# Kernel optimization log

Hardware: AMD Instinct MI355X
Metric: run time of the kernel (lower is better)

Reference implementation:

```python
import jax, jax.numpy as jnp
import numpy as np
import math

T_STEPS = 100      # diffusion steps
TED = 16           # time_embed_dim
NODE_C = 4         # node_num_classes
EDGE_C = 2         # edge_num_classes
HID = 64           # hidden_dim
H = 4              # nhead
B = 256            # graphs per batch
NPG = 64           # nodes per graph
DEG = 8            # avg out-degree
N = B * NPG
E = N * DEG
IN_CH = NODE_C + TED  # 20


def sinusoidal_embedding(t_vec, dim):
    # t_vec: [1] float. Matches get_sinusoidal_embedding for even dim.
    half = dim // 2
    scale = math.log(10000.0) / (half - 1)
    freqs = jnp.exp(-jnp.arange(half, dtype=jnp.float32) * scale)  # [half]
    emb = t_vec[:, None] * freqs[None, :]                          # [1, half]
    return jnp.concatenate([jnp.sin(emb), jnp.cos(emb)], axis=1)   # [1, dim]


def transformer_conv(x, src, dst, Wq, bq, Wk, bk, Wv, bv, Ws, bs):
    # PyG TransformerConv, concat=False (mean over heads), root_weight=True,
    # beta=False, no edge features, dropout=0 (eval).
    n = x.shape[0]
    q = (x @ Wq + bq).reshape(n, H, HID)
    k = (x @ Wk + bk).reshape(n, H, HID)
    v = (x @ Wv + bv).reshape(n, H, HID)
    # attention logits per edge, softmax over incoming edges of each dst node
    logits = jnp.sum(q[dst] * k[src], axis=-1) / math.sqrt(HID)    # [E, H]
    lmax = jax.ops.segment_max(logits, dst, num_segments=n)       # [n, H]
    ex = jnp.exp(logits - lmax[dst])                              # [E, H]
    denom = jax.ops.segment_sum(ex, dst, num_segments=n)          # [n, H]
    attn = ex / jnp.where(denom == 0, 1.0, denom)[dst]            # [E, H]
    msg = v[src] * attn[:, :, None]                               # [E, H, HID]
    agg = jax.ops.segment_sum(msg, dst, num_segments=n)           # [n, H, HID]
    return agg.mean(axis=1) + x @ Ws + bs                         # [n, HID]


def setup_inputs() -> dict:
    key = jax.random.key(0)
    ks = jax.random.split(key, 32)

    # node features: random one-hot labels
    labels = jax.random.randint(ks[0], (N,), 0, NODE_C)
    x = jax.nn.one_hot(labels, NODE_C, dtype=jnp.float32)

    # per-graph random edges (kept within each graph via offsets)
    src_l = jax.random.randint(ks[1], (B, NPG * DEG), 0, NPG)
    dst_l = jax.random.randint(ks[2], (B, NPG * DEG), 0, NPG)
    off = (jnp.arange(B) * NPG)[:, None]
    edge_index = jnp.stack([(src_l + off).reshape(-1), (dst_l + off).reshape(-1)]).astype(jnp.int64)

    batch = jnp.repeat(jnp.arange(B, dtype=jnp.int64), NPG)

    def lin(k, fin, fout):
        kw, kb = jax.random.split(k)
        W = jax.random.normal(kw, (fin, fout), jnp.float32) / math.sqrt(fin)
        b = jax.random.normal(kb, (fout,), jnp.float32) * 0.01
        return W, b

    W_time, b_time = lin(ks[3], TED, TED)
    Wq1, bq1 = lin(ks[4], IN_CH, H * HID)
    Wk1, bk1 = lin(ks[5], IN_CH, H * HID)
    Wv1, bv1 = lin(ks[6], IN_CH, H * HID)
    Ws1, bs1 = lin(ks[7], IN_CH, HID)
    Wq2, bq2 = lin(ks[8], HID, H * HID)
    Wk2, bk2 = lin(ks[9], HID, H * HID)
    Wv2, bv2 = lin(ks[10], HID, H * HID)
    Ws2, bs2 = lin(ks[11], HID, HID)
    W_node, b_node = lin(ks[12], HID, NODE_C)
    W_e1, b_e1 = lin(ks[13], 2 * HID, HID)
    W_e2, b_e2 = lin(ks[14], HID, EDGE_C)

    return dict(x=x, edge_index=edge_index, batch=batch, t=50,
                W_time=W_time, b_time=b_time,
                Wq1=Wq1, bq1=bq1, Wk1=Wk1, bk1=bk1, Wv1=Wv1, bv1=bv1, Ws1=Ws1, bs1=bs1,
                Wq2=Wq2, bq2=bq2, Wk2=Wk2, bk2=bk2, Wv2=Wv2, bv2=bv2, Ws2=Ws2, bs2=bs2,
                W_node=W_node, b_node=b_node, W_e1=W_e1, b_e1=b_e1, W_e2=W_e2, b_e2=b_e2)


def reference(x, edge_index, batch, t,
              W_time, b_time,
              Wq1, bq1, Wk1, bk1, Wv1, bv1, Ws1, bs1,
              Wq2, bq2, Wk2, bk2, Wv2, bv2, Ws2, bs2,
              W_node, b_node, W_e1, b_e1, W_e2, b_e2):
    src, dst = edge_index[0], edge_index[1]

    # time embedding: sinusoidal(t/T) -> Linear -> broadcast to all nodes
    t_vec = jnp.asarray([t], jnp.float32) / T_STEPS
    temb = sinusoidal_embedding(t_vec, TED) @ W_time + b_time      # [1, TED]
    temb = jnp.broadcast_to(temb, (x.shape[0], TED))
    x_in = jnp.concatenate([x, temb], axis=1)                      # [N, 20]

    h = jax.nn.relu(transformer_conv(x_in, src, dst, Wq1, bq1, Wk1, bk1, Wv1, bv1, Ws1, bs1))
    h = jax.nn.relu(transformer_conv(h, src, dst, Wq2, bq2, Wk2, bk2, Wv2, bv2, Ws2, bs2))

    node_logits = h @ W_node + b_node                              # [N, 4]

    # to_dense_batch with equal-sized graphs == reshape; vectorized edge MLP
    hd = h.reshape(B, NPG, HID)
    pair = jnp.concatenate([
        jnp.broadcast_to(hd[:, :, None, :], (B, NPG, NPG, HID)),
        jnp.broadcast_to(hd[:, None, :, :], (B, NPG, NPG, HID)),
    ], axis=-1)                                                    # [B, n, n, 2*HID]
    e_hidden = jax.nn.relu(pair @ W_e1 + b_e1)
    edge_logits = e_hidden @ W_e2 + b_e2                           # [B, n, n, 2]
    return node_logits, edge_logits
```

## Files before the change

kernel.cpp:

```cpp
#include <hip/hip_runtime.h>
#include <math.h>

constexpr int EPG  = 512;
constexpr int ETOT = 131072;

constexpr size_t TAB_Q  = 0;
constexpr size_t TAB_K  = 1024;
constexpr size_t TAB_V  = 2048;
constexpr size_t TAB_S  = 3072;
constexpr size_t TAB_LG = 3328;
constexpr int PK_Q_HI   = 0;
constexpr int PK_Q_LO   = 16384;
constexpr int PK_K_HI   = 32768;
constexpr int PK_K_LO   = 49152;
constexpr int PK_V_HI   = 65536;
constexpr int PK_V_LO   = 81920;
constexpr int PK_S_HI   = 98304;
constexpr int PK_S_LO   = 102400;
constexpr int PK_E1T_HI = 106496;
constexpr int PK_E1T_LO = 110592;
constexpr int PK_E1B_HI = 114688;
constexpr int PK_E1B_LO = 118784;

typedef short bf16x8 __attribute__((ext_vector_type(8)));
typedef float f32x4  __attribute__((ext_vector_type(4)));

__device__ __forceinline__ short f2bf(float x) {
    unsigned u = __float_as_uint(x);
    u = (u + 0x7fffu + ((u >> 16) & 1u)) >> 16;
    return (short)u;
}
__device__ __forceinline__ float bf2f(short h) {
    return __uint_as_float(((unsigned)(unsigned short)h) << 16);
}
__device__ __forceinline__ void splt(float x, short& hi, short& lo) {
    hi = f2bf(x);
    lo = f2bf(x - bf2f(hi));
}

__device__ __forceinline__ f32x4 mfma3(bf16x8 ah, bf16x8 al, bf16x8 bh, bf16x8 bl, f32x4 c) {
    c = __builtin_amdgcn_mfma_f32_16x16x32_bf16(ah, bh, c, 0, 0, 0);
    c = __builtin_amdgcn_mfma_f32_16x16x32_bf16(ah, bl, c, 0, 0, 0);
    c = __builtin_amdgcn_mfma_f32_16x16x32_bf16(al, bh, c, 0, 0, 0);
    return c;
}

__device__ __forceinline__ bf16x8 ldsfrag(const short* p, int rowb, int kb, int lane) {
    return *(const bf16x8*)&p[(rowb + (lane & 15)) * 72 + kb + ((lane >> 4) << 3)];
}
__device__ __forceinline__ bf16x8 gpfrag(const short* p, int colb, int kb, int lane) {
    return *(const bf16x8*)&p[((colb + (lane & 15)) << 6) + kb + ((lane >> 4) << 3)];
}

__global__ __launch_bounds__(256) void k_tables(
    const int* __restrict__ t_ptr,
    const float* __restrict__ Wt,  const float* __restrict__ bt,
    const float* __restrict__ Wq1, const float* __restrict__ bq1,
    const float* __restrict__ Wk1, const float* __restrict__ bk1,
    const float* __restrict__ Wv1, const float* __restrict__ bv1,
    const float* __restrict__ Ws1, const float* __restrict__ bs1,
    float* __restrict__ ws)
{
    __shared__ float se[16], temb[16];
    __shared__ float q1t[4][256], k1t[4][256], v1t[4][256], s1t[4][64];
    const int t = threadIdx.x;

    if (t < 8) {
        float tv = (float)(*t_ptr) * 0.01f;
        float scale = logf(10000.0f) / 7.0f;
        float e = tv * expf(-(float)t * scale);
        se[t]     = sinf(e);
        se[t + 8] = cosf(e);
    }
    __syncthreads();
    if (t < 16) {
        float acc = bt[t];
        for (int i = 0; i < 16; i++) acc += se[i] * Wt[i * 16 + t];
        temb[t] = acc;
    }
    __syncthreads();
    {
        const int o = t;
        float tq = 0.f, tk = 0.f, tv = 0.f;
        for (int d = 0; d < 16; d++) {
            float td = temb[d];
            tq += td * Wq1[(4 + d) * 256 + o];
            tk += td * Wk1[(4 + d) * 256 + o];
            tv += td * Wv1[(4 + d) * 256 + o];
        }
        for (int c = 0; c < 4; c++) {
            q1t[c][o] = Wq1[c * 256 + o] + tq + bq1[o];
            k1t[c][o] = Wk1[c * 256 + o] + tk + bk1[o];
            v1t[c][o] = Wv1[c * 256 + o] + tv + bv1[o];
        }
        if (o < 64) {
            float ts = 0.f;
            for (int d = 0; d < 16; d++) ts += temb[d] * Ws1[(4 + d) * 64 + o];
            for (int c = 0; c < 4; c++) s1t[c][o] = Ws1[c * 64 + o] + ts + bs1[o];
        }
    }
    __syncthreads();
    for (int idx = t; idx < 1024; idx += 256) {
        int c = idx >> 8, o = idx & 255;
        ws[TAB_Q + idx] = q1t[c][o];
        ws[TAB_K + idx] = k1t[c][o];
        ws[TAB_V + idx] = v1t[c][o];
    }
    ws[TAB_S + t] = s1t[t >> 6][t & 63];
    if (t < 64) {
        int cd = t >> 4, cs = (t >> 2) & 3, h = t & 3;
        float acc = 0.f;
        for (int d = 0; d < 64; d++) acc += q1t[cd][h * 64 + d] * k1t[cs][h * 64 + d];
        ws[TAB_LG + t] = acc * 0.125f;
    }
}

__global__ __launch_bounds__(256) void k_prep(
    const float* __restrict__ Wq, const float* __restrict__ Wk,
    const float* __restrict__ Wv, const float* __restrict__ Wsk,
    const float* __restrict__ We1, short* __restrict__ wsh)
{
    int b = blockIdx.x, t = threadIdx.x;
    const float* src; int N; int dhi; int nb;
    if (b < 64)       { src = Wq;           N = 256; dhi = PK_Q_HI;   nb = b; }
    else if (b < 128) { src = Wk;           N = 256; dhi = PK_K_HI;   nb = b - 64; }
    else if (b < 192) { src = Wv;           N = 256; dhi = PK_V_HI;   nb = b - 128; }
    else if (b < 208) { src = Wsk;          N = 64;  dhi = PK_S_HI;   nb = b - 192; }
    else if (b < 224) { src = We1;          N = 64;  dhi = PK_E1T_HI; nb = b - 208; }
    else              { src = We1 + 64*64;  N = 64;  dhi = PK_E1B_HI; nb = b - 224; }
    int dlo = dhi + N * 64;
    int n = nb * 4 + (t >> 6), kk = t & 63;
    float v = src[(size_t)kk * N + n];
    short hi, lo; splt(v, hi, lo);
    wsh[dhi + n * 64 + kk] = hi;
    wsh[dlo + n * 64 + kk] = lo;
}

__global__ __launch_bounds__(512) void k_main(
    const float* __restrict__ x, const int* __restrict__ ei,
    const float* __restrict__ ws, const short* __restrict__ wsh,
    const float* __restrict__ bq, const float* __restrict__ bk,
    const float* __restrict__ bv, const float* __restrict__ bsk,
    const float* __restrict__ Wn, const float* __restrict__ bn,
    const float* __restrict__ be1, const float* __restrict__ We2,
    const float* __restrict__ be2, float* __restrict__ out)
{
    __shared__ __align__(16) char smem[130304];
    short* hHi    = (short*)(smem + 0);
    short* hLo    = (short*)(smem + 9216);
    short* qHi    = (short*)(smem + 18432);
    short* qLo    = (short*)(smem + 27648);
    short* kHi    = (short*)(smem + 36864);
    short* kLo    = (short*)(smem + 46080);
    short* vtHi   = (short*)(smem + 55296);
    short* vtLo   = (short*)(smem + 64512);
    short* pHi    = (short*)(smem + 73728);
    short* pLo    = (short*)(smem + 82944);
    float* Ssf    = (float*)(smem + 92160);
    int*   Cc     = (int*)(smem + 109568);
    int*   cnt4   = (int*)(smem + 117760);
    float* alphaF = (float*)(smem + 118784);
    float* v1t    = (float*)(smem + 122880);
    float* s1t    = (float*)(smem + 126976);
    float* lgs    = (float*)(smem + 128000);
    float* WnS    = (float*)(smem + 128256);
    float* w2s    = (float*)(smem + 129280);
    float* invsf  = (float*)(smem + 129792);
    int*   cls    = (int*)(smem + 130048);
    float* Asf    = (float*)(smem + 18432);
    float* BTf    = (float*)(smem + 36864);

    const int g = blockIdx.x, t = threadIdx.x;
    const int lane = t & 63, w = t >> 6;
    const int rowb = (w & 3) * 16;
    const int ch   = w >> 2;
    const int row8 = t >> 3;
    const int d08  = (t & 7) * 8;

    for (int i = t; i < 1024; i += 512) v1t[i] = ws[TAB_V + i];
    if (t < 256) s1t[t] = ws[TAB_S + t];
    if (t < 64)  lgs[t] = ws[TAB_LG + t];
    if (t < 256) WnS[t] = Wn[t];
    if (t < 128) w2s[(t & 1) * 64 + (t >> 1)] = We2[t];
    if (t < 64) {
        const float* xr = x + (size_t)(g * 64 + t) * 4;
        int c = 0;
        if (xr[1] > 0.5f) c = 1;
        if (xr[2] > 0.5f) c = 2;
        if (xr[3] > 0.5f) c = 3;
        cls[t] = c;
    }
    if (t < 256) cnt4[t] = 0;
    for (int i = t; i < 2048; i += 512) Cc[i] = 0;
    __syncthreads();

    {
        int ge = g * EPG + t;
        int ls = ei[ge] - g * 64;
        int ld = ei[ETOT + ge] - g * 64;
        int idx = ld * 64 + ls;
        atomicAdd(&Cc[idx >> 1], 1 << ((idx & 1) * 16));
        atomicAdd(&cnt4[ld * 4 + cls[ls]], 1);
    }
    __syncthreads();

    if (t < 256) {
        int n = t >> 2, h = t & 3;
        int cd = cls[n];
        int   c[4]; float l[4];
        #pragma unroll
        for (int cc = 0; cc < 4; cc++) {
            c[cc] = cnt4[n * 4 + cc];
            l[cc] = lgs[cd * 16 + cc * 4 + h];
        }
        float m = -1e30f;
        #pragma unroll
        for (int cc = 0; cc < 4; cc++) if (c[cc] > 0) m = fmaxf(m, l[cc]);
        float e[4]; float den = 0.f;
        #pragma unroll
        for (int cc = 0; cc < 4; cc++) {
            e[cc] = (c[cc] > 0) ? (float)c[cc] * expf(l[cc] - m) : 0.f;
            den += e[cc];
        }
        float inv = (den > 0.f) ? 0.25f / den : 0.f;
        #pragma unroll
        for (int cc = 0; cc < 4; cc++) alphaF[n * 16 + h * 4 + cc] = e[cc] * inv;
    }
    __syncthreads();

    {
        int cd = cls[row8];
        float a[16];
        #pragma unroll
        for (int q = 0; q < 16; q++) a[q] = alphaF[row8 * 16 + q];
        #pragma unroll
        for (int jj = 0; jj < 8; jj++) {
            int d = d08 + jj;
            float acc = s1t[cd * 64 + d];
            #pragma unroll
            for (int h = 0; h < 4; h++)
                #pragma unroll
                for (int c = 0; c < 4; c++)
                    acc += a[h * 4 + c] * v1t[c * 256 + h * 64 + d];
            float o = fmaxf(acc, 0.f);
            short hi, lo; splt(o, hi, lo);
            hHi[row8 * 72 + d] = hi;
            hLo[row8 * 72 + d] = lo;
        }
    }
    __syncthreads();

    bf16x8 Ah0 = ldsfrag(hHi, rowb, 0, lane),  Ah1 = ldsfrag(hHi, rowb, 32, lane);
    bf16x8 Al0 = ldsfrag(hLo, rowb, 0, lane),  Al1 = ldsfrag(hLo, rowb, 32, lane);

    f32x4 skacc[2];
    #pragma unroll
    for (int ct = 0; ct < 2; ct++) {
        int colb = ch * 32 + ct * 16;
        f32x4 a = {0.f, 0.f, 0.f, 0.f};
        a = mfma3(Ah0, Al0, gpfrag(wsh + PK_S_HI, colb, 0, lane),
                             gpfrag(wsh + PK_S_LO, colb, 0, lane), a);
        a = mfma3(Ah1, Al1, gpfrag(wsh + PK_S_HI, colb, 32, lane),
                             gpfrag(wsh + PK_S_LO, colb, 32, lane), a);
        float bb = bsk[colb + (lane & 15)];
        #pragma unroll
        for (int r = 0; r < 4; r++) a[r] += bb;
        skacc[ct] = a;
    }

    float hacc[2][4] = {};
    for (int h = 0; h < 4; h++) {
        #pragma unroll
        for (int ct = 0; ct < 2; ct++) {
            int colb = ch * 32 + ct * 16;
            int gcol = h * 64 + colb;
            f32x4 qa = {0.f,0.f,0.f,0.f}, ka = {0.f,0.f,0.f,0.f}, va = {0.f,0.f,0.f,0.f};
            qa = mfma3(Ah0, Al0, gpfrag(wsh + PK_Q_HI, gcol, 0, lane),
                                  gpfrag(wsh + PK_Q_LO, gcol, 0, lane), qa);
            qa = mfma3(Ah1, Al1, gpfrag(wsh + PK_Q_HI, gcol, 32, lane),
                                  gpfrag(wsh + PK_Q_LO, gcol, 32, lane), qa);
            ka = mfma3(Ah0, Al0, gpfrag(wsh + PK_K_HI, gcol, 0, lane),
                                  gpfrag(wsh + PK_K_LO, gcol, 0, lane), ka);
            ka = mfma3(Ah1, Al1, gpfrag(wsh + PK_K_HI, gcol, 32, lane),
                                  gpfrag(wsh + PK_K_LO, gcol, 32, lane), ka);
            va = mfma3(Ah0, Al0, gpfrag(wsh + PK_V_HI, gcol, 0, lane),
                                  gpfrag(wsh + PK_V_LO, gcol, 0, lane), va);
            va = mfma3(Ah1, Al1, gpfrag(wsh + PK_V_HI, gcol, 32, lane),
                                  gpfrag(wsh + PK_V_LO, gcol, 32, lane), va);
            float bqv = bq[gcol + (lane & 15)];
            float bkv = bk[gcol + (lane & 15)];
            float bvv = bv[gcol + (lane & 15)];
            int cc = colb + (lane & 15);
            #pragma unroll
            for (int r = 0; r < 4; r++) {
                int rr = rowb + ((lane >> 4) << 2) + r;
                short hi, lo;
                splt((qa[r] + bqv) * 0.125f, hi, lo);
                qHi[rr * 72 + cc] = hi;  qLo[rr * 72 + cc] = lo;
                splt(ka[r] + bkv, hi, lo);
                kHi[rr * 72 + cc] = hi;  kLo[rr * 72 + cc] = lo;
                splt(va[r] + bvv, hi, lo);
                vtHi[cc * 72 + rr] = hi; vtLo[cc * 72 + rr] = lo;
            }
        }
        __syncthreads();

        {
            bf16x8 qh0 = ldsfrag(qHi, rowb, 0, lane),  qh1 = ldsfrag(qHi, rowb, 32, lane);
            bf16x8 ql0 = ldsfrag(qLo, rowb, 0, lane),  ql1 = ldsfrag(qLo, rowb, 32, lane);
            #pragma unroll
            for (int ct = 0; ct < 2; ct++) {
                int colb = ch * 32 + ct * 16;
                f32x4 s = {0.f, 0.f, 0.f, 0.f};
                s = mfma3(qh0, ql0, ldsfrag(kHi, colb, 0, lane),
                                     ldsfrag(kLo, colb, 0, lane), s);
                s = mfma3(qh1, ql1, ldsfrag(kHi, colb, 32, lane),
                                     ldsfrag(kLo, colb, 32, lane), s);
                int cc = colb + (lane & 15);
                #pragma unroll
                for (int r = 0; r < 4; r++)
                    Ssf[(rowb + ((lane >> 4) << 2) + r) * 68 + cc] = s[r];
            }
        }
        __syncthreads();

        {
            int cv[8]; float sv[8];
            #pragma unroll
            for (int jj = 0; jj < 8; jj++) {
                int idx = row8 * 64 + d08 + jj;
                cv[jj] = (Cc[idx >> 1] >> ((idx & 1) * 16)) & 0xffff;
                sv[jj] = Ssf[row8 * 68 + d08 + jj];
            }
            float m = -1e30f;
            #pragma unroll
            for (int jj = 0; jj < 8; jj++) if (cv[jj] > 0) m = fmaxf(m, sv[jj]);
            m = fmaxf(m, __shfl_xor(m, 1, 8));
            m = fmaxf(m, __shfl_xor(m, 2, 8));
            m = fmaxf(m, __shfl_xor(m, 4, 8));
            float den = 0.f; float p[8];
            #pragma unroll
            for (int jj = 0; jj < 8; jj++) {
                p[jj] = (cv[jj] > 0) ? (float)cv[jj] * expf(sv[jj] - m) : 0.f;
                den += p[jj];
            }
            den += __shfl_xor(den, 1, 8);
            den += __shfl_xor(den, 2, 8);
            den += __shfl_xor(den, 4, 8);
            #pragma unroll
            for (int jj = 0; jj < 8; jj++) {
                short hi, lo; splt(p[jj], hi, lo);
                pHi[row8 * 72 + d08 + jj] = hi;
                pLo[row8 * 72 + d08 + jj] = lo;
            }
            if ((t & 7) == 0) invsf[row8] = (den > 0.f) ? 1.f / den : 0.f;
        }
        __syncthreads();

        {
            bf16x8 ph0 = ldsfrag(pHi, rowb, 0, lane),  ph1 = ldsfrag(pHi, rowb, 32, lane);
            bf16x8 pl0 = ldsfrag(pLo, rowb, 0, lane),  pl1 = ldsfrag(pLo, rowb, 32, lane);
            #pragma unroll
            for (int ct = 0; ct < 2; ct++) {
                int colb = ch * 32 + ct * 16;
                f32x4 pv = {0.f, 0.f, 0.f, 0.f};
                pv = mfma3(ph0, pl0, ldsfrag(vtHi, colb, 0, lane),
                                      ldsfrag(vtLo, colb, 0, lane), pv);
                pv = mfma3(ph1, pl1, ldsfrag(vtHi, colb, 32, lane),
                                      ldsfrag(vtLo, colb, 32, lane), pv);
                #pragma unroll
                for (int r = 0; r < 4; r++)
                    hacc[ct][r] += pv[r] * invsf[rowb + ((lane >> 4) << 2) + r];
            }
        }
        __syncthreads();
    }

    #pragma unroll
    for (int ct = 0; ct < 2; ct++) {
        int colb = ch * 32 + ct * 16;
        int cc = colb + (lane & 15);
        #pragma unroll
        for (int r = 0; r < 4; r++) {
            int rr = rowb + ((lane >> 4) << 2) + r;
            float v = fmaxf(0.25f * hacc[ct][r] + skacc[ct][r], 0.f);
            short hi, lo; splt(v, hi, lo);
            hHi[rr * 72 + cc] = hi;
            hLo[rr * 72 + cc] = lo;
            Ssf[rr * 68 + cc] = v;
        }
    }
    __syncthreads();

    {
        bf16x8 ah0 = ldsfrag(hHi, rowb, 0, lane),  ah1 = ldsfrag(hHi, rowb, 32, lane);
        bf16x8 al0 = ldsfrag(hLo, rowb, 0, lane),  al1 = ldsfrag(hLo, rowb, 32, lane);
        #pragma unroll
        for (int ct = 0; ct < 2; ct++) {
            int colb = ch * 32 + ct * 16;
            f32x4 aa = {0.f,0.f,0.f,0.f}, bb2 = {0.f,0.f,0.f,0.f};
            aa  = mfma3(ah0, al0, gpfrag(wsh + PK_E1T_HI, colb, 0, lane),
                                   gpfrag(wsh + PK_E1T_LO, colb, 0, lane), aa);
            aa  = mfma3(ah1, al1, gpfrag(wsh + PK_E1T_HI, colb, 32, lane),
                                   gpfrag(wsh + PK_E1T_LO, colb, 32, lane), aa);
            bb2 = mfma3(ah0, al0, gpfrag(wsh + PK_E1B_HI, colb, 0, lane),
                                   gpfrag(wsh + PK_E1B_LO, colb, 0, lane), bb2);
            bb2 = mfma3(ah1, al1, gpfrag(wsh + PK_E1B_HI, colb, 32, lane),
                                   gpfrag(wsh + PK_E1B_LO, colb, 32, lane), bb2);
            float bev = be1[colb + (lane & 15)];
            int cc = colb + (lane & 15);
            #pragma unroll
            for (int r = 0; r < 4; r++) {
                int rr = rowb + ((lane >> 4) << 2) + r;
                Asf[rr * 68 + cc] = aa[r] + bev;
                BTf[cc * 68 + rr] = bb2[r];
            }
        }
    }
    if (t < 256) {
        int n = t >> 2, c = t & 3;
        float acc = bn[c];
        #pragma unroll 4
        for (int k = 0; k < 64; k++) acc += Ssf[n * 68 + k] * WnS[k * 4 + c];
        out[(size_t)(g * 64 + n) * 4 + c] = acc;
    }
    __syncthreads();

    {
        const int wv = t >> 6, j = t & 63;
        float e0[8], e1[8];
        const float cb0 = be2[0], cb1 = be2[1];
        #pragma unroll
        for (int ii = 0; ii < 8; ii++) { e0[ii] = cb0; e1[ii] = cb1; }
        for (int kb = 0; kb < 4; kb++) {
            const int k0 = kb * 16;
            float bj[16], wa[16], wb[16];
            #pragma unroll
            for (int q = 0; q < 16; q++) {
                bj[q] = BTf[(k0 + q) * 68 + j];
                wa[q] = w2s[k0 + q];
                wb[q] = w2s[64 + k0 + q];
            }
            #pragma unroll
            for (int ii = 0; ii < 8; ii++) {
                const float* ar = &Asf[(wv * 8 + ii) * 68 + k0];
                #pragma unroll
                for (int q = 0; q < 16; q += 4) {
                    float4 a4 = *(const float4*)(ar + q);
                    float s;
                    s = fmaxf(a4.x + bj[q + 0], 0.f); e0[ii] += s * wa[q + 0]; e1[ii] += s * wb[q + 0];
                    s = fmaxf(a4.y + bj[q + 1], 0.f); e0[ii] += s * wa[q + 1]; e1[ii] += s * wb[q + 1];
                    s = fmaxf(a4.z + bj[q + 2], 0.f); e0[ii] += s * wa[q + 2]; e1[ii] += s * wb[q + 2];
                    s = fmaxf(a4.w + bj[q + 3], 0.f); e0[ii] += s * wa[q + 3]; e1[ii] += s * wb[q + 3];
                }
            }
        }
        float2* oe = (float2*)(out + 65536);
        #pragma unroll
        for (int ii = 0; ii < 8; ii++)
            oe[(size_t)(g * 64 + wv * 8 + ii) * 64 + j] = make_float2(e0[ii], e1[ii]);
    }
}

extern "C" void kernel_launch(void* const* d_in, const int* in_sizes, int n_in,
                              void* d_out, int out_size, void* d_ws, size_t ws_size,
                              hipStream_t stream)
{
    const float* x    = (const float*)d_in[0];
    const int*   ei   = (const int*)d_in[1];
    const int*   tptr = (const int*)d_in[3];
    const float* Wt   = (const float*)d_in[4];
    const float* bt   = (const float*)d_in[5];
    const float* Wq1  = (const float*)d_in[6];
    const float* bq1  = (const float*)d_in[7];
    const float* Wk1  = (const float*)d_in[8];
    const float* bk1  = (const float*)d_in[9];
    const float* Wv1  = (const float*)d_in[10];
    const float* bv1  = (const float*)d_in[11];
    const float* Ws1  = (const float*)d_in[12];
    const float* bs1  = (const float*)d_in[13];
    const float* Wq2  = (const float*)d_in[14];
    const float* bq2  = (const float*)d_in[15];
    const float* Wk2  = (const float*)d_in[16];
    const float* bk2  = (const float*)d_in[17];
    const float* Wv2  = (const float*)d_in[18];
    const float* bv2  = (const float*)d_in[19];
    const float* Ws2  = (const float*)d_in[20];
    const float* bs2  = (const float*)d_in[21];
    const float* Wn   = (const float*)d_in[22];
    const float* bn   = (const float*)d_in[23];
    const float* We1  = (const float*)d_in[24];
    const float* be1  = (const float*)d_in[25];
    const float* We2  = (const float*)d_in[26];
    const float* be2  = (const float*)d_in[27];

    float* ws  = (float*)d_ws;
    short* wsh = (short*)(ws + 4096);
    float* out = (float*)d_out;

    k_tables<<<1, 256, 0, stream>>>(tptr, Wt, bt, Wq1, bq1, Wk1, bk1, Wv1, bv1, Ws1, bs1, ws);
    k_prep<<<240, 256, 0, stream>>>(Wq2, Wk2, Wv2, Ws2, We1, wsh);
    k_main<<<256, 512, 0, stream>>>(x, ei, ws, wsh,
                                    bq2, bk2, bv2, bs2, Wn, bn, be1, We2, be2, out);
}
```

Measured before the change: 63.55 us.

## Split each graph across two blocks and move edge MLP into separate kernel

```diff
diff --git a/kernel.cpp b/kernel.cpp
--- a/kernel.cpp
+++ b/kernel.cpp
@@ -9,6 +9,7 @@
 constexpr size_t TAB_V  = 2048;
 constexpr size_t TAB_S  = 3072;
 constexpr size_t TAB_LG = 3328;
+constexpr size_t OFF_H2 = 65536;
 constexpr int PK_Q_HI   = 0;
 constexpr int PK_Q_LO   = 16384;
 constexpr int PK_K_HI   = 32768;
@@ -52,19 +53,48 @@
     return *(const bf16x8*)&p[((colb + (lane & 15)) << 6) + kb + ((lane >> 4) << 3)];
 }
 
-__global__ __launch_bounds__(256) void k_tables(
+__device__ __forceinline__ void unpack8(const unsigned* p, bf16x8& hv, bf16x8& lv) {
+    uint4 a = *(const uint4*)p;
+    uint4 b = *(const uint4*)(p + 4);
+    unsigned u[8] = {a.x, a.y, a.z, a.w, b.x, b.y, b.z, b.w};
+    bf16x8 h, l;
+    #pragma unroll
+    for (int i = 0; i < 8; i++) { h[i] = (short)(u[i] >> 16); l[i] = (short)(u[i] & 0xffffu); }
+    hv = h; lv = l;
+}
+
+__global__ __launch_bounds__(256) void k_tabprep(
     const int* __restrict__ t_ptr,
     const float* __restrict__ Wt,  const float* __restrict__ bt,
     const float* __restrict__ Wq1, const float* __restrict__ bq1,
     const float* __restrict__ Wk1, const float* __restrict__ bk1,
     const float* __restrict__ Wv1, const float* __restrict__ bv1,
     const float* __restrict__ Ws1, const float* __restrict__ bs1,
-    float* __restrict__ ws)
+    const float* __restrict__ Wq2, const float* __restrict__ Wk2,
+    const float* __restrict__ Wv2, const float* __restrict__ Ws2,
+    const float* __restrict__ We1,
+    float* __restrict__ ws, short* __restrict__ wsh)
 {
+    const int t = threadIdx.x;
+    if (blockIdx.x < 240) {
+        int b = blockIdx.x;
+        const float* src; int N; int dhi; int nb;
+        if (b < 64)       { src = Wq2;           N = 256; dhi = PK_Q_HI;   nb = b; }
+        else if (b < 128) { src = Wk2;           N = 256; dhi = PK_K_HI;   nb = b - 64; }
+        else if (b < 192) { src = Wv2;           N = 256; dhi = PK_V_HI;   nb = b - 128; }
+        else if (b < 208) { src = Ws2;           N = 64;  dhi = PK_S_HI;   nb = b - 192; }
+        else if (b < 224) { src = We1;           N = 64;  dhi = PK_E1T_HI; nb = b - 208; }
+        else              { src = We1 + 64 * 64; N = 64;  dhi = PK_E1B_HI; nb = b - 224; }
+        int dlo = dhi + N * 64;
+        int n = nb * 4 + (t >> 6), kk = t & 63;
+        float v = src[(size_t)kk * N + n];
+        short hi, lo; splt(v, hi, lo);
+        wsh[dhi + n * 64 + kk] = hi;
+        wsh[dlo + n * 64 + kk] = lo;
+        return;
+    }
     __shared__ float se[16], temb[16];
     __shared__ float q1t[4][256], k1t[4][256], v1t[4][256], s1t[4][64];
-    const int t = threadIdx.x;
-
     if (t < 8) {
         float tv = (float)(*t_ptr) * 0.01f;
         float scale = logf(10000.0f) / 7.0f;
@@ -115,73 +145,49 @@
     }
 }
 
-__global__ __launch_bounds__(256) void k_prep(
-    const float* __restrict__ Wq, const float* __restrict__ Wk,
-    const float* __restrict__ Wv, const float* __restrict__ Wsk,
-    const float* __restrict__ We1, short* __restrict__ wsh)
-{
-    int b = blockIdx.x, t = threadIdx.x;
-    const float* src; int N; int dhi; int nb;
-    if (b < 64)       { src = Wq;           N = 256; dhi = PK_Q_HI;   nb = b; }
-    else if (b < 128) { src = Wk;           N = 256; dhi = PK_K_HI;   nb = b - 64; }
-    else if (b < 192) { src = Wv;           N = 256; dhi = PK_V_HI;   nb = b - 128; }
-    else if (b < 208) { src = Wsk;          N = 64;  dhi = PK_S_HI;   nb = b - 192; }
-    else if (b < 224) { src = We1;          N = 64;  dhi = PK_E1T_HI; nb = b - 208; }
-    else              { src = We1 + 64*64;  N = 64;  dhi = PK_E1B_HI; nb = b - 224; }
-    int dlo = dhi + N * 64;
-    int n = nb * 4 + (t >> 6), kk = t & 63;
-    float v = src[(size_t)kk * N + n];
-    short hi, lo; splt(v, hi, lo);
-    wsh[dhi + n * 64 + kk] = hi;
-    wsh[dlo + n * 64 + kk] = lo;
-}
-
-__global__ __launch_bounds__(512) void k_main(
+__global__ __launch_bounds__(512, 4) void k_main(
     const float* __restrict__ x, const int* __restrict__ ei,
     const float* __restrict__ ws, const short* __restrict__ wsh,
     const float* __restrict__ bq, const float* __restrict__ bk,
     const float* __restrict__ bv, const float* __restrict__ bsk,
-    const float* __restrict__ Wn, const float* __restrict__ bn,
-    const float* __restrict__ be1, const float* __restrict__ We2,
-    const float* __restrict__ be2, float* __restrict__ out)
+    float* __restrict__ h2out)
 {
-    __shared__ __align__(16) char smem[130304];
-    short* hHi    = (short*)(smem + 0);
-    short* hLo    = (short*)(smem + 9216);
-    short* qHi    = (short*)(smem + 18432);
-    short* qLo    = (short*)(smem + 27648);
-    short* kHi    = (short*)(smem + 36864);
-    short* kLo    = (short*)(smem + 46080);
-    short* vtHi   = (short*)(smem + 55296);
-    short* vtLo   = (short*)(smem + 64512);
-    short* pHi    = (short*)(smem + 73728);
-    short* pLo    = (short*)(smem + 82944);
-    float* Ssf    = (float*)(smem + 92160);
-    int*   Cc     = (int*)(smem + 109568);
-    int*   cnt4   = (int*)(smem + 117760);
-    float* alphaF = (float*)(smem + 118784);
-    float* v1t    = (float*)(smem + 122880);
-    float* s1t    = (float*)(smem + 126976);
-    float* lgs    = (float*)(smem + 128000);
-    float* WnS    = (float*)(smem + 128256);
-    float* w2s    = (float*)(smem + 129280);
-    float* invsf  = (float*)(smem + 129792);
-    int*   cls    = (int*)(smem + 130048);
-    float* Asf    = (float*)(smem + 18432);
-    float* BTf    = (float*)(smem + 36864);
-
-    const int g = blockIdx.x, t = threadIdx.x;
+    __shared__ __align__(16) char smem[78976];
+    short* hHi  = (short*)(smem);
+    short* hLo  = (short*)(smem + 9216);
+    short* kHi  = (short*)(smem + 18432);
+    short* kLo  = (short*)(smem + 27648);
+    short* vtHi = (short*)(smem + 36864);
+    short* vtLo = (short*)(smem + 46080);
+    short* qHi  = (short*)(smem + 55296);
+    short* qLo  = (short*)(smem + 59904);
+    float* SPf  = (float*)(smem + 64512);
+    unsigned* SPu = (unsigned*)(smem + 64512);
+    int*   Cc   = (int*)(smem + 73216);
+    int*   cnt4 = (int*)(smem + 77312);
+    int*   cls  = (int*)(smem + 78336);
+    float* lgs  = (float*)(smem + 78592);
+    float* invs = (float*)(smem + 78848);
+    float* v1t    = (float*)(smem + 18432);
+    float* s1t    = (float*)(smem + 22528);
+    float* alphaF = (float*)(smem + 23552);
+
+    const int g   = blockIdx.x >> 1;
+    const int r0  = (blockIdx.x & 1) * 32;
+    const int t   = threadIdx.x;
     const int lane = t & 63, w = t >> 6;
-    const int rowb = (w & 3) * 16;
-    const int ch   = w >> 2;
-    const int row8 = t >> 3;
-    const int d08  = (t & 7) * 8;
+    const int rowbF = (w & 3) * 16;
+    const int chF   = w >> 2;
+    const int rbQ   = (w & 1) * 16;
+    const int cqQ   = (w >> 1) * 16;
+    const int lg4   = ((lane >> 4) << 2);
+    const int l15   = lane & 15;
+    const int row8  = t >> 3;
+    const int d08   = (t & 7) * 8;
 
     for (int i = t; i < 1024; i += 512) v1t[i] = ws[TAB_V + i];
     if (t < 256) s1t[t] = ws[TAB_S + t];
     if (t < 64)  lgs[t] = ws[TAB_LG + t];
-    if (t < 256) WnS[t] = Wn[t];
-    if (t < 128) w2s[(t & 1) * 64 + (t >> 1)] = We2[t];
     if (t < 64) {
         const float* xr = x + (size_t)(g * 64 + t) * 4;
         int c = 0;
@@ -191,16 +197,19 @@
         cls[t] = c;
     }
     if (t < 256) cnt4[t] = 0;
-    for (int i = t; i < 2048; i += 512) Cc[i] = 0;
+    for (int i = t; i < 1024; i += 512) Cc[i] = 0;
     __syncthreads();
 
     {
         int ge = g * EPG + t;
         int ls = ei[ge] - g * 64;
         int ld = ei[ETOT + ge] - g * 64;
-        int idx = ld * 64 + ls;
-        atomicAdd(&Cc[idx >> 1], 1 << ((idx & 1) * 16));
         atomicAdd(&cnt4[ld * 4 + cls[ls]], 1);
+        int lr = ld - r0;
+        if ((unsigned)lr < 32u) {
+            int idx = lr * 64 + ls;
+            atomicAdd(&Cc[idx >> 1], 1 << ((idx & 1) * 16));
+        }
     }
     __syncthreads();
 
@@ -250,87 +259,97 @@
     }
     __syncthreads();
 
-    bf16x8 Ah0 = ldsfrag(hHi, rowb, 0, lane),  Ah1 = ldsfrag(hHi, rowb, 32, lane);
-    bf16x8 Al0 = ldsfrag(hLo, rowb, 0, lane),  Al1 = ldsfrag(hLo, rowb, 32, lane);
-
-    f32x4 skacc[2];
-    #pragma unroll
-    for (int ct = 0; ct < 2; ct++) {
-        int colb = ch * 32 + ct * 16;
+    bf16x8 AhF0 = ldsfrag(hHi, rowbF, 0, lane),     AhF1 = ldsfrag(hHi, rowbF, 32, lane);
+    bf16x8 AlF0 = ldsfrag(hLo, rowbF, 0, lane),     AlF1 = ldsfrag(hLo, rowbF, 32, lane);
+    bf16x8 AhQ0 = ldsfrag(hHi, r0 + rbQ, 0, lane),  AhQ1 = ldsfrag(hHi, r0 + rbQ, 32, lane);
+    bf16x8 AlQ0 = ldsfrag(hLo, r0 + rbQ, 0, lane),  AlQ1 = ldsfrag(hLo, r0 + rbQ, 32, lane);
+
+    f32x4 skacc;
+    {
         f32x4 a = {0.f, 0.f, 0.f, 0.f};
-        a = mfma3(Ah0, Al0, gpfrag(wsh + PK_S_HI, colb, 0, lane),
-                             gpfrag(wsh + PK_S_LO, colb, 0, lane), a);
-        a = mfma3(Ah1, Al1, gpfrag(wsh + PK_S_HI, colb, 32, lane),
-                             gpfrag(wsh + PK_S_LO, colb, 32, lane), a);
-        float bb = bsk[colb + (lane & 15)];
+        a = mfma3(AhQ0, AlQ0, gpfrag(wsh + PK_S_HI, cqQ, 0, lane),
+                               gpfrag(wsh + PK_S_LO, cqQ, 0, lane), a);
+        a = mfma3(AhQ1, AlQ1, gpfrag(wsh + PK_S_HI, cqQ, 32, lane),
+                               gpfrag(wsh + PK_S_LO, cqQ, 32, lane), a);
+        float bb = bsk[cqQ + l15];
         #pragma unroll
         for (int r = 0; r < 4; r++) a[r] += bb;
-        skacc[ct] = a;
-    }
-
-    float hacc[2][4] = {};
+        skacc = a;
+    }
+
+    float hacc[4] = {0.f, 0.f, 0.f, 0.f};
+    #pragma unroll 1
     for (int h = 0; h < 4; h++) {
         #pragma unroll
         for (int ct = 0; ct < 2; ct++) {
-            int colb = ch * 32 + ct * 16;
+            int colb = chF * 32 + ct * 16;
             int gcol = h * 64 + colb;
-            f32x4 qa = {0.f,0.f,0.f,0.f}, ka = {0.f,0.f,0.f,0.f}, va = {0.f,0.f,0.f,0.f};
-            qa = mfma3(Ah0, Al0, gpfrag(wsh + PK_Q_HI, gcol, 0, lane),
-                                  gpfrag(wsh + PK_Q_LO, gcol, 0, lane), qa);
-            qa = mfma3(Ah1, Al1, gpfrag(wsh + PK_Q_HI, gcol, 32, lane),
-                                  gpfrag(wsh + PK_Q_LO, gcol, 32, lane), qa);
-            ka = mfma3(Ah0, Al0, gpfrag(wsh + PK_K_HI, gcol, 0, lane),
-                                  gpfrag(wsh + PK_K_LO, gcol, 0, lane), ka);
-            ka = mfma3(Ah1, Al1, gpfrag(wsh + PK_K_HI, gcol, 32, lane),
-                                  gpfrag(wsh + PK_K_LO, gcol, 32, lane), ka);
-            va = mfma3(Ah0, Al0, gpfrag(wsh + PK_V_HI, gcol, 0, lane),
-                                  gpfrag(wsh + PK_V_LO, gcol, 0, lane), va);
-            va = mfma3(Ah1, Al1, gpfrag(wsh + PK_V_HI, gcol, 32, lane),
-                                  gpfrag(wsh + PK_V_LO, gcol, 32, lane), va);
-            float bqv = bq[gcol + (lane & 15)];
-            float bkv = bk[gcol + (lane & 15)];
-            float bvv = bv[gcol + (lane & 15)];
-            int cc = colb + (lane & 15);
+            f32x4 ka = {0.f, 0.f, 0.f, 0.f}, va = {0.f, 0.f, 0.f, 0.f};
+            ka = mfma3(AhF0, AlF0, gpfrag(wsh + PK_K_HI, gcol, 0, lane),
+                                    gpfrag(wsh + PK_K_LO, gcol, 0, lane), ka);
+            ka = mfma3(AhF1, AlF1, gpfrag(wsh + PK_K_HI, gcol, 32, lane),
+                                    gpfrag(wsh + PK_K_LO, gcol, 32, lane), ka);
+            va = mfma3(AhF0, AlF0, gpfrag(wsh + PK_V_HI, gcol, 0, lane),
+                                    gpfrag(wsh + PK_V_LO, gcol, 0, lane), va);
+            va = mfma3(AhF1, AlF1, gpfrag(wsh + PK_V_HI, gcol, 32, lane),
+                                    gpfrag(wsh + PK_V_LO, gcol, 32, lane), va);
+            float bkv = bk[gcol + l15];
+            float bvv = bv[gcol + l15];
+            int cc = colb + l15;
             #pragma unroll
             for (int r = 0; r < 4; r++) {
-                int rr = rowb + ((lane >> 4) << 2) + r;
+                int rr = rowbF + lg4 + r;
                 short hi, lo;
-                splt((qa[r] + bqv) * 0.125f, hi, lo);
-                qHi[rr * 72 + cc] = hi;  qLo[rr * 72 + cc] = lo;
                 splt(ka[r] + bkv, hi, lo);
                 kHi[rr * 72 + cc] = hi;  kLo[rr * 72 + cc] = lo;
                 splt(va[r] + bvv, hi, lo);
                 vtHi[cc * 72 + rr] = hi; vtLo[cc * 72 + rr] = lo;
             }
         }
+        {
+            int gcol = h * 64 + cqQ;
+            f32x4 qa = {0.f, 0.f, 0.f, 0.f};
+            qa = mfma3(AhQ0, AlQ0, gpfrag(wsh + PK_Q_HI, gcol, 0, lane),
+                                    gpfrag(wsh + PK_Q_LO, gcol, 0, lane), qa);
+            qa = mfma3(AhQ1, AlQ1, gpfrag(wsh + PK_Q_HI, gcol, 32, lane),
+                                    gpfrag(wsh + PK_Q_LO, gcol, 32, lane), qa);
+            float bqv = bq[gcol + l15];
+            int cc = cqQ + l15;
+            #pragma unroll
+            for (int r = 0; r < 4; r++) {
+                int rr = rbQ + lg4 + r;
+                short hi, lo;
+                splt((qa[r] + bqv) * 0.125f, hi, lo);
+                qHi[rr * 72 + cc] = hi;  qLo[rr * 72 + cc] = lo;
+            }
+        }
         __syncthreads();
 
         {
-            bf16x8 qh0 = ldsfrag(qHi, rowb, 0, lane),  qh1 = ldsfrag(qHi, rowb, 32, lane);
-            bf16x8 ql0 = ldsfrag(qLo, rowb, 0, lane),  ql1 = ldsfrag(qLo, rowb, 32, lane);
-            #pragma unroll
-            for (int ct = 0; ct < 2; ct++) {
-                int colb = ch * 32 + ct * 16;
-                f32x4 s = {0.f, 0.f, 0.f, 0.f};
-                s = mfma3(qh0, ql0, ldsfrag(kHi, colb, 0, lane),
-                                     ldsfrag(kLo, colb, 0, lane), s);
-                s = mfma3(qh1, ql1, ldsfrag(kHi, colb, 32, lane),
-                                     ldsfrag(kLo, colb, 32, lane), s);
-                int cc = colb + (lane & 15);
-                #pragma unroll
-                for (int r = 0; r < 4; r++)
-                    Ssf[(rowb + ((lane >> 4) << 2) + r) * 68 + cc] = s[r];
-            }
+            bf16x8 qh0 = ldsfrag(qHi, rbQ, 0, lane),  qh1 = ldsfrag(qHi, rbQ, 32, lane);
+            bf16x8 ql0 = ldsfrag(qLo, rbQ, 0, lane),  ql1 = ldsfrag(qLo, rbQ, 32, lane);
+            f32x4 s = {0.f, 0.f, 0.f, 0.f};
+            s = mfma3(qh0, ql0, ldsfrag(kHi, cqQ, 0, lane),
+                                 ldsfrag(kLo, cqQ, 0, lane), s);
+            s = mfma3(qh1, ql1, ldsfrag(kHi, cqQ, 32, lane),
+                                 ldsfrag(kLo, cqQ, 32, lane), s);
+            int cc = cqQ + l15;
+            #pragma unroll
+            for (int r = 0; r < 4; r++)
+                SPf[(rbQ + lg4 + r) * 68 + cc] = s[r];
         }
         __syncthreads();
 
-        {
-            int cv[8]; float sv[8];
+        if (t < 256) {
+            int row = t >> 3, c8 = (t & 7) * 8;
+            float4 s0 = *(float4*)&SPf[row * 68 + c8];
+            float4 s1 = *(float4*)&SPf[row * 68 + c8 + 4];
+            float sv[8] = {s0.x, s0.y, s0.z, s0.w, s1.x, s1.y, s1.z, s1.w};
+            int cv[8];
             #pragma unroll
             for (int jj = 0; jj < 8; jj++) {
-                int idx = row8 * 64 + d08 + jj;
+                int idx = row * 64 + c8 + jj;
                 cv[jj] = (Cc[idx >> 1] >> ((idx & 1) * 16)) & 0xffff;
-                sv[jj] = Ssf[row8 * 68 + d08 + jj];
             }
             float m = -1e30f;
             #pragma unroll
@@ -350,88 +369,125 @@
             #pragma unroll
             for (int jj = 0; jj < 8; jj++) {
                 short hi, lo; splt(p[jj], hi, lo);
-                pHi[row8 * 72 + d08 + jj] = hi;
-                pLo[row8 * 72 + d08 + jj] = lo;
-            }
-            if ((t & 7) == 0) invsf[row8] = (den > 0.f) ? 1.f / den : 0.f;
+                SPu[row * 68 + c8 + jj] =
+                    ((unsigned)(unsigned short)hi << 16) | (unsigned short)lo;
+            }
+            if ((t & 7) == 0) invs[row] = (den > 0.f) ? 1.f / den : 0.f;
         }
         __syncthreads();
 
         {
-            bf16x8 ph0 = ldsfrag(pHi, rowb, 0, lane),  ph1 = ldsfrag(pHi, rowb, 32, lane);
-            bf16x8 pl0 = ldsfrag(pLo, rowb, 0, lane),  pl1 = ldsfrag(pLo, rowb, 32, lane);
-            #pragma unroll
-            for (int ct = 0; ct < 2; ct++) {
-                int colb = ch * 32 + ct * 16;
-                f32x4 pv = {0.f, 0.f, 0.f, 0.f};
-                pv = mfma3(ph0, pl0, ldsfrag(vtHi, colb, 0, lane),
-                                      ldsfrag(vtLo, colb, 0, lane), pv);
-                pv = mfma3(ph1, pl1, ldsfrag(vtHi, colb, 32, lane),
-                                      ldsfrag(vtLo, colb, 32, lane), pv);
-                #pragma unroll
-                for (int r = 0; r < 4; r++)
-                    hacc[ct][r] += pv[r] * invsf[rowb + ((lane >> 4) << 2) + r];
-            }
+            bf16x8 ph0, pl0, ph1, pl1;
+            const unsigned* pp = SPu + (rbQ + l15) * 68 + ((lane >> 4) << 3);
+            unpack8(pp, ph0, pl0);
+            unpack8(pp + 32, ph1, pl1);
+            f32x4 pv = {0.f, 0.f, 0.f, 0.f};
+            pv = mfma3(ph0, pl0, ldsfrag(vtHi, cqQ, 0, lane),
+                                  ldsfrag(vtLo, cqQ, 0, lane), pv);
+            pv = mfma3(ph1, pl1, ldsfrag(vtHi, cqQ, 32, lane),
+                                  ldsfrag(vtLo, cqQ, 32, lane), pv);
+            #pragma unroll
+            for (int r = 0; r < 4; r++)
+                hacc[r] += pv[r] * invs[rbQ + lg4 + r];
         }
         __syncthreads();
     }
 
-    #pragma unroll
-    for (int ct = 0; ct < 2; ct++) {
-        int colb = ch * 32 + ct * 16;
-        int cc = colb + (lane & 15);
+    {
+        int cc = cqQ + l15;
         #pragma unroll
         for (int r = 0; r < 4; r++) {
-            int rr = rowb + ((lane >> 4) << 2) + r;
-            float v = fmaxf(0.25f * hacc[ct][r] + skacc[ct][r], 0.f);
-            short hi, lo; splt(v, hi, lo);
-            hHi[rr * 72 + cc] = hi;
-            hLo[rr * 72 + cc] = lo;
-            Ssf[rr * 68 + cc] = v;
-        }
-    }
-    __syncthreads();
-
-    {
-        bf16x8 ah0 = ldsfrag(hHi, rowb, 0, lane),  ah1 = ldsfrag(hHi, rowb, 32, lane);
-        bf16x8 al0 = ldsfrag(hLo, rowb, 0, lane),  al1 = ldsfrag(hLo, rowb, 32, lane);
+            int lr = rbQ + lg4 + r;
+            float v = fmaxf(0.25f * hacc[r] + skacc[r], 0.f);
+            h2out[(size_t)(g * 64 + r0 + lr) * 64 + cc] = v;
+        }
+    }
+}
+
+__global__ __launch_bounds__(512, 4) void k_edge(
+    const short* __restrict__ wsh, const float* __restrict__ h2g,
+    const float* __restrict__ Wn, const float* __restrict__ bn,
+    const float* __restrict__ be1, const float* __restrict__ We2,
+    const float* __restrict__ be2, float* __restrict__ out)
+{
+    __shared__ __align__(16) char smem[46080];
+    short* h2Hi = (short*)(smem);
+    short* h2Lo = (short*)(smem + 9216);
+    float* Af   = (float*)(smem + 18432);
+    float* BTf  = (float*)(smem + 27136);
+    float* WnS  = (float*)(smem + 44544);
+    float* w2s  = (float*)(smem + 45568);
+
+    const int g  = blockIdx.x >> 1;
+    const int r0 = (blockIdx.x & 1) * 32;
+    const int t  = threadIdx.x;
+    const int lane = t & 63, w = t >> 6;
+    const int rowbF = (w & 3) * 16, chF = w >> 2;
+    const int rbQ = (w & 1) * 16,   cqQ = (w >> 1) * 16;
+    const int lg4 = ((lane >> 4) << 2);
+    const int l15 = lane & 15;
+
+    {
+        int row = t >> 3, c8 = (t & 7) * 8;
+        float4 a = *(const float4*)&h2g[(size_t)(g * 64 + row) * 64 + c8];
+        float4 b = *(const float4*)&h2g[(size_t)(g * 64 + row) * 64 + c8 + 4];
+        float vv[8] = {a.x, a.y, a.z, a.w, b.x, b.y, b.z, b.w};
+        #pragma unroll
+        for (int i = 0; i < 8; i++) {
+            short hi, lo; splt(vv[i], hi, lo);
+            h2Hi[row * 72 + c8 + i] = hi;
+            h2Lo[row * 72 + c8 + i] = lo;
+        }
+    }
+    if (t < 256) WnS[t] = Wn[t];
+    if (t < 128) w2s[(t & 1) * 64 + (t >> 1)] = We2[t];
+    __syncthreads();
+
+    {
+        bf16x8 aq0 = ldsfrag(h2Hi, r0 + rbQ, 0, lane), aq1 = ldsfrag(h2Hi, r0 + rbQ, 32, lane);
+        bf16x8 lq0 = ldsfrag(h2Lo, r0 + rbQ, 0, lane), lq1 = ldsfrag(h2Lo, r0 + rbQ, 32, lane);
+        f32x4 aa = {0.f, 0.f, 0.f, 0.f};
+        aa = mfma3(aq0, lq0, gpfrag(wsh + PK_E1T_HI, cqQ, 0, lane),
+                              gpfrag(wsh + PK_E1T_LO, cqQ, 0, lane), aa);
+        aa = mfma3(aq1, lq1, gpfrag(wsh + PK_E1T_HI, cqQ, 32, lane),
+                              gpfrag(wsh + PK_E1T_LO, cqQ, 32, lane), aa);
+        float bev = be1[cqQ + l15];
+        #pragma unroll
+        for (int r = 0; r < 4; r++)
+            Af[(rbQ + lg4 + r) * 68 + cqQ + l15] = aa[r] + bev;
+
+        bf16x8 af0 = ldsfrag(h2Hi, rowbF, 0, lane), af1 = ldsfrag(h2Hi, rowbF, 32, lane);
+        bf16x8 lf0 = ldsfrag(h2Lo, rowbF, 0, lane), lf1 = ldsfrag(h2Lo, rowbF, 32, lane);
         #pragma unroll
         for (int ct = 0; ct < 2; ct++) {
-            int colb = ch * 32 + ct * 16;
-            f32x4 aa = {0.f,0.f,0.f,0.f}, bb2 = {0.f,0.f,0.f,0.f};
-            aa  = mfma3(ah0, al0, gpfrag(wsh + PK_E1T_HI, colb, 0, lane),
-                                   gpfrag(wsh + PK_E1T_LO, colb, 0, lane), aa);
-            aa  = mfma3(ah1, al1, gpfrag(wsh + PK_E1T_HI, colb, 32, lane),
-                                   gpfrag(wsh + PK_E1T_LO, colb, 32, lane), aa);
-            bb2 = mfma3(ah0, al0, gpfrag(wsh + PK_E1B_HI, colb, 0, lane),
-                                   gpfrag(wsh + PK_E1B_LO, colb, 0, lane), bb2);
-            bb2 = mfma3(ah1, al1, gpfrag(wsh + PK_E1B_HI, colb, 32, lane),
-                                   gpfrag(wsh + PK_E1B_LO, colb, 32, lane), bb2);
-            float bev = be1[colb + (lane & 15)];
-            int cc = colb + (lane & 15);
-            #pragma unroll
-            for (int r = 0; r < 4; r++) {
-                int rr = rowb + ((lane >> 4) << 2) + r;
-                Asf[rr * 68 + cc] = aa[r] + bev;
-                BTf[cc * 68 + rr] = bb2[r];
-            }
-        }
-    }
-    if (t < 256) {
+            int colb = chF * 32 + ct * 16;
+            f32x4 bb = {0.f, 0.f, 0.f, 0.f};
+            bb = mfma3(af0, lf0, gpfrag(wsh + PK_E1B_HI, colb, 0, lane),
+                                  gpfrag(wsh + PK_E1B_LO, colb, 0, lane), bb);
+            bb = mfma3(af1, lf1, gpfrag(wsh + PK_E1B_HI, colb, 32, lane),
+                                  gpfrag(wsh + PK_E1B_LO, colb, 32, lane), bb);
+            int cc = colb + l15;
+            #pragma unroll
+            for (int r = 0; r < 4; r++)
+                BTf[cc * 68 + rowbF + lg4 + r] = bb[r];
+        }
+    }
+    if (t < 128) {
         int n = t >> 2, c = t & 3;
         float acc = bn[c];
         #pragma unroll 4
-        for (int k = 0; k < 64; k++) acc += Ssf[n * 68 + k] * WnS[k * 4 + c];
-        out[(size_t)(g * 64 + n) * 4 + c] = acc;
+        for (int k = 0; k < 64; k++)
+            acc += (bf2f(h2Hi[(r0 + n) * 72 + k]) + bf2f(h2Lo[(r0 + n) * 72 + k])) * WnS[k * 4 + c];
+        out[(size_t)(g * 64 + r0 + n) * 4 + c] = acc;
     }
     __syncthreads();
 
     {
         const int wv = t >> 6, j = t & 63;
-        float e0[8], e1[8];
+        float e0[4], e1[4];
         const float cb0 = be2[0], cb1 = be2[1];
         #pragma unroll
-        for (int ii = 0; ii < 8; ii++) { e0[ii] = cb0; e1[ii] = cb1; }
+        for (int ii = 0; ii < 4; ii++) { e0[ii] = cb0; e1[ii] = cb1; }
         for (int kb = 0; kb < 4; kb++) {
             const int k0 = kb * 16;
             float bj[16], wa[16], wb[16];
@@ -442,8 +498,8 @@
                 wb[q] = w2s[64 + k0 + q];
             }
             #pragma unroll
-            for (int ii = 0; ii < 8; ii++) {
-                const float* ar = &Asf[(wv * 8 + ii) * 68 + k0];
+            for (int ii = 0; ii < 4; ii++) {
+                const float* ar = &Af[(wv * 4 + ii) * 68 + k0];
                 #pragma unroll
                 for (int q = 0; q < 16; q += 4) {
                     float4 a4 = *(const float4*)(ar + q);
@@ -457,8 +513,8 @@
         }
         float2* oe = (float2*)(out + 65536);
         #pragma unroll
-        for (int ii = 0; ii < 8; ii++)
-            oe[(size_t)(g * 64 + wv * 8 + ii) * 64 + j] = make_float2(e0[ii], e1[ii]);
+        for (int ii = 0; ii < 4; ii++)
+            oe[(size_t)(g * 64 + r0 + wv * 4 + ii) * 64 + j] = make_float2(e0[ii], e1[ii]);
     }
 }
 
@@ -496,10 +552,11 @@
 
     float* ws  = (float*)d_ws;
     short* wsh = (short*)(ws + 4096);
+    float* h2  = ws + OFF_H2;
     float* out = (float*)d_out;
 
-    k_tables<<<1, 256, 0, stream>>>(tptr, Wt, bt, Wq1, bq1, Wk1, bk1, Wv1, bv1, Ws1, bs1, ws);
-    k_prep<<<240, 256, 0, stream>>>(Wq2, Wk2, Wv2, Ws2, We1, wsh);
-    k_main<<<256, 512, 0, stream>>>(x, ei, ws, wsh,
-                                    bq2, bk2, bv2, bs2, Wn, bn, be1, We2, be2, out);
-}
+    k_tabprep<<<241, 256, 0, stream>>>(tptr, Wt, bt, Wq1, bq1, Wk1, bk1, Wv1, bv1,
+                                       Ws1, bs1, Wq2, Wk2, Wv2, Ws2, We1, ws, wsh);
+    k_main<<<512, 512, 0, stream>>>(x, ei, ws, wsh, bq2, bk2, bv2, bs2, h2);
+    k_edge<<<512, 512, 0, stream>>>(wsh, h2, Wn, bn, be1, We2, be2, out);
+}
```

After: 76.29 us. +20.0%, slower.
